# Kernel optimization log

Measured on AMD Instinct MI355X. Metric: run time of the kernel, lower is better.

## Reference

```python
import jax, jax.numpy as jnp
import numpy as np

B, T, D, N, K, H = 2, 2048, 2560, 8, 4, 256
G = N // K
WINDOW = 1024
ROPE_BASE = 10000
K_MASK = -2.3819763e+38
EPS = 1e-6


def apply_rope(inputs, positions, base_frequency):
    # inputs: [B, L, n, H]; positions: [B, L]
    head_dim = inputs.shape[-1]
    fraction = 2 * jnp.arange(0, head_dim // 2) / head_dim
    timescale = base_frequency ** fraction
    sinusoid = positions[..., None] / timescale[None, None, :]   # [B, L, H/2]
    sinusoid = sinusoid[..., None, :]                            # [B, L, 1, H/2]
    sin, cos = jnp.sin(sinusoid), jnp.cos(sinusoid)
    first, second = jnp.split(inputs, 2, axis=-1)
    out = jnp.concatenate([first * cos - second * sin,
                           second * cos + first * sin], axis=-1)
    return out.astype(inputs.dtype)


def rms_norm(x, scale):
    # Gemma-style RMSNorm: normalize over last dim, (1 + scale) gain.
    var = jnp.mean(jnp.square(x), axis=-1, keepdims=True)
    return x * jax.lax.rsqrt(var + EPS) * (1.0 + scale)


def setup_inputs() -> dict:
    key = jax.random.key(0)
    ks = jax.random.split(key, 5)
    x = jax.random.normal(ks[0], (B, T, D), jnp.float32)
    positions = jnp.broadcast_to(jnp.arange(T, dtype=jnp.int32), (B, T))
    # Causal sliding-window mask (LOCAL_SLIDING, window=1024), shape [B, 1, T, S].
    qp = jnp.arange(T)[:, None]
    kp = jnp.arange(T)[None, :]
    mask = (kp <= qp) & ((qp - kp) < WINDOW)
    attn_mask = jnp.broadcast_to(mask[None, None], (B, 1, T, T))
    q_w = jax.random.normal(ks[1], (N, D, H), jnp.float32) * 0.02
    kv_w = jax.random.normal(ks[2], (2, K, D, H), jnp.float32) * 0.02
    q_scale = jnp.zeros((H,), jnp.float32)
    k_scale = jnp.zeros((H,), jnp.float32)
    out_w = jax.random.normal(ks[3], (N, H, D), jnp.float32) * 0.02
    return {"x": x, "q_w": q_w, "kv_w": kv_w, "q_scale": q_scale,
            "k_scale": k_scale, "out_w": out_w,
            "positions": positions, "attn_mask": attn_mask}


def reference(x, q_w, kv_w, q_scale, k_scale, out_w, positions, attn_mask):
    dtype = x.dtype
    # GQA projections (num_kv_heads != num_heads branch)
    q = jnp.einsum('BTD,NDH->BTNH', x, q_w)          # [B,T,N,H]
    k = jnp.einsum('BSD,KDH->BSKH', x, kv_w[0])      # [B,S,K,H]
    v = jnp.einsum('BSD,KDH->BSKH', x, kv_w[1])      # [B,S,K,H]
    # QK-RMSNorm (GQA branch only)
    q = rms_norm(q, q_scale)
    k = rms_norm(k, k_scale)
    # RoPE + query scaling
    q = apply_rope(q, positions, ROPE_BASE)
    q = q * (H ** -0.5)
    k = apply_rope(k, positions, ROPE_BASE)
    # Grouped attention logits: [B,T,K,G,S] -> [B,T,N,S]
    qg = q.reshape(B, T, K, G, H)
    logits = jnp.einsum('BTKGH,BSKH->BTKGS', qg, k)
    logits = logits.reshape(B, T, N, T)
    # Mask + softmax (mask [B,1,T,S] -> [B,T,1,S])
    bmask = jnp.expand_dims(attn_mask.squeeze(axis=1), axis=2)
    masked = jnp.where(bmask, logits, K_MASK)
    probs = jax.nn.softmax(masked, axis=-1).astype(dtype)
    # Weighted values with grouped kv heads
    pg = probs.reshape(B, T, K, G, T)
    enc = jnp.einsum('BTKGS,BSKH->BTKGH', pg, v).reshape(B, T, N, H)
    out = jnp.einsum('BTNH,NHD->BTD', enc, out_w)
    return out
```

## Files before the change

### kernel.cpp

```cpp
#include <hip/hip_runtime.h>
#include <cstdint>

#define TB 2048
#define DIM 2560
#define NQ 8
#define NKV 4
#define HDIM 256
#define WIN 1024
#define KMASK -2.3819763e+38f

using f32x4 = __attribute__((ext_vector_type(4))) float;
using s16x8 = __attribute__((ext_vector_type(8))) short;
using u16x4 = __attribute__((ext_vector_type(4))) unsigned short;

__device__ __forceinline__ unsigned short f2bf(float f) {
  uint32_t x = __builtin_bit_cast(uint32_t, f);
  x += 0x7FFFu + ((x >> 16) & 1u);
  return (unsigned short)(x >> 16);
}

__device__ __forceinline__ float bf2f(unsigned short u) {
  uint32_t x = (uint32_t)u << 16;
  return __builtin_bit_cast(float, x);
}

__global__ __launch_bounds__(256) void k_prep(const float* __restrict__ q_w,
                                              const float* __restrict__ kv_w,
                                              const float* __restrict__ out_w,
                                              const float* __restrict__ x,
                                              unsigned short* __restrict__ W1,
                                              unsigned short* __restrict__ W3,
                                              unsigned short* __restrict__ XB) {
  __shared__ float tile[32][33];
  const int bi = blockIdx.x;
  const int tid = threadIdx.x;
  if (bi < 10240) {
    const int hd = bi / 640;
    const int rem = bi % 640;
    const int r0 = (rem / 8) * 32, c0 = (rem % 8) * 32;
    const float* src = (hd < 8) ? (q_w + (size_t)hd * DIM * HDIM)
                                : (kv_w + (size_t)(hd - 8) * DIM * HDIM);
    unsigned short* dst = W1 + (size_t)hd * HDIM * DIM;
    const int tx = tid & 31, ty = tid >> 5;
#pragma unroll
    for (int i = 0; i < 32; i += 8)
      tile[ty + i][tx] = src[(size_t)(r0 + ty + i) * HDIM + c0 + tx];
    __syncthreads();
#pragma unroll
    for (int i = 0; i < 32; i += 8)
      dst[(size_t)(c0 + ty + i) * DIM + r0 + tx] = f2bf(tile[tx][ty + i]);
  } else if (bi < 15360) {
    const int j = bi - 10240;
    const int c0 = (j % 80) * 32, r0 = (j / 80) * 32;
    const int tx = tid & 31, ty = tid >> 5;
#pragma unroll
    for (int i = 0; i < 32; i += 8)
      tile[ty + i][tx] = out_w[(size_t)(r0 + ty + i) * DIM + c0 + tx];
    __syncthreads();
#pragma unroll
    for (int i = 0; i < 32; i += 8)
      W3[(size_t)(c0 + ty + i) * 2048 + r0 + tx] = f2bf(tile[tx][ty + i]);
  } else {
    const int j = bi - 15360;
    int i = j * 256 + tid;
    f32x4 v = *(const f32x4*)&x[(size_t)i * 4];
    u16x4 o;
#pragma unroll
    for (int k = 0; k < 4; ++k) o[k] = f2bf(v[k]);
    *(u16x4*)&XB[(size_t)i * 4] = o;
  }
}

__global__ __launch_bounds__(512, 2) void k_gemm(const unsigned short* __restrict__ A,
                                                 const unsigned short* __restrict__ Bw,
                                                 void* __restrict__ Cc,
                                                 int Nc, int Kd, int nxl, int bf16out) {
  __shared__ unsigned short shA[2][256 * 64];
  __shared__ unsigned short shB[2][256 * 64];
  const int tid = threadIdx.x, w = tid >> 6, l = tid & 63;
  const int xcd = blockIdx.x & 7, loc = blockIdx.x >> 3;
  const int m0 = ((xcd >> 1) * 4 + loc / nxl) * 256;
  const int n0 = ((xcd & 1) * nxl + loc % nxl) * 256;

  const int srow = l >> 3;
  const int sw_colb = (((l & 7) ^ srow) << 4);
  const int wrow = w * 8;
  const int NT = Kd >> 6;

#define STG_A(buf, t, r)                                                                     \
  {                                                                                          \
    const char* src_ = (const char*)A +                                                      \
        ((size_t)(m0 + (r) * 64 + wrow + srow) * Kd + ((size_t)(t) << 6)) * 2 + sw_colb;     \
    __builtin_amdgcn_global_load_lds(                                                        \
        (__attribute__((address_space(1))) void*)src_,                                       \
        (__attribute__((address_space(3))) void*)((char*)&shA[buf][0] + (r) * 8192 + w * 1024), \
        16, 0, 0);                                                                           \
  }
#define STG_B(buf, t, r)                                                                     \
  {                                                                                          \
    const char* src_ = (const char*)Bw +                                                     \
        ((size_t)(n0 + (r) * 64 + wrow + srow) * Kd + ((size_t)(t) << 6)) * 2 + sw_colb;     \
    __builtin_amdgcn_global_load_lds(                                                        \
        (__attribute__((address_space(1))) void*)src_,                                       \
        (__attribute__((address_space(3))) void*)((char*)&shB[buf][0] + (r) * 8192 + w * 1024), \
        16, 0, 0);                                                                           \
  }

  const int wm = w >> 2, wn = w & 3;
  const int lr = l & 15, lg = l >> 4;
  const int rswz = (lr & 7) << 4;
  const int c0x = (lg * 16) ^ rswz;
  const int c1x = (64 + lg * 16) ^ rswz;
  f32x4 acc[8][4] = {};

#pragma unroll
  for (int r = 0; r < 4; ++r) { STG_A(0, 0, r); STG_B(0, 0, r); }
  asm volatile("s_waitcnt vmcnt(0)" ::: "memory");
  __builtin_amdgcn_s_barrier();

#pragma unroll 2
  for (int t = 0; t < NT; ++t) {
    const int buf = t & 1;
    const bool pf = (t + 1 < NT);
    const char* sa = (const char*)&shA[buf][0];
    const char* sb = (const char*)&shB[buf][0];
    s16x8 af[4], bf0[4], bf1[4];

#pragma unroll
    for (int mi = 0; mi < 4; ++mi)
      af[mi] = *(const s16x8*)(sa + (wm * 128 + mi * 16 + lr) * 128 + c0x);
#pragma unroll
    for (int ni = 0; ni < 4; ++ni)
      bf0[ni] = *(const s16x8*)(sb + (wn * 64 + ni * 16 + lr) * 128 + c0x);
    asm volatile("s_waitcnt vmcnt(0)" ::: "memory");
    if (pf) { STG_A(buf ^ 1, t + 1, 0); STG_A(buf ^ 1, t + 1, 2); }
    __builtin_amdgcn_s_barrier();
    asm volatile("s_waitcnt lgkmcnt(0)" ::: "memory");
    __builtin_amdgcn_s_setprio(1);
#pragma unroll
    for (int mi = 0; mi < 4; ++mi)
#pragma unroll
      for (int ni = 0; ni < 4; ++ni)
        acc[mi][ni] = __builtin_amdgcn_mfma_f32_16x16x32_bf16(af[mi], bf0[ni], acc[mi][ni], 0, 0, 0);
    __builtin_amdgcn_s_setprio(0);
    __builtin_amdgcn_s_barrier();

#pragma unroll
    for (int mi = 0; mi < 4; ++mi)
      af[mi] = *(const s16x8*)(sa + (wm * 128 + (4 + mi) * 16 + lr) * 128 + c0x);
    if (pf) { STG_B(buf ^ 1, t + 1, 0); STG_B(buf ^ 1, t + 1, 1); }
    __builtin_amdgcn_s_barrier();
    asm volatile("s_waitcnt lgkmcnt(0)" ::: "memory");
    __builtin_amdgcn_s_setprio(1);
#pragma unroll
    for (int mi = 0; mi < 4; ++mi)
#pragma unroll
      for (int ni = 0; ni < 4; ++ni)
        acc[4 + mi][ni] = __builtin_amdgcn_mfma_f32_16x16x32_bf16(af[mi], bf0[ni], acc[4 + mi][ni], 0, 0, 0);
    __builtin_amdgcn_s_setprio(0);
    __builtin_amdgcn_s_barrier();

#pragma unroll
    for (int mi = 0; mi < 4; ++mi)
      af[mi] = *(const s16x8*)(sa + (wm * 128 + mi * 16 + lr) * 128 + c1x);
#pragma unroll
    for (int ni = 0; ni < 4; ++ni)
      bf1[ni] = *(const s16x8*)(sb + (wn * 64 + ni * 16 + lr) * 128 + c1x);
    if (pf) { STG_B(buf ^ 1, t + 1, 2); STG_B(buf ^ 1, t + 1, 3); }
    __builtin_amdgcn_s_barrier();
    asm volatile("s_waitcnt lgkmcnt(0)" ::: "memory");
    __builtin_amdgcn_s_setprio(1);
#pragma unroll
    for (int mi = 0; mi < 4; ++mi)
#pragma unroll
      for (int ni = 0; ni < 4; ++ni)
        acc[mi][ni] = __builtin_amdgcn_mfma_f32_16x16x32_bf16(af[mi], bf1[ni], acc[mi][ni], 0, 0, 0);
    __builtin_amdgcn_s_setprio(0);
    __builtin_amdgcn_s_barrier();

#pragma unroll
    for (int mi = 0; mi < 4; ++mi)
      af[mi] = *(const s16x8*)(sa + (wm * 128 + (4 + mi) * 16 + lr) * 128 + c1x);
    if (pf) { STG_A(buf ^ 1, t + 1, 1); STG_A(buf ^ 1, t + 1, 3); }
    __builtin_amdgcn_s_barrier();
    asm volatile("s_waitcnt lgkmcnt(0)" ::: "memory");
    __builtin_amdgcn_s_setprio(1);
#pragma unroll
    for (int mi = 0; mi < 4; ++mi)
#pragma unroll
      for (int ni = 0; ni < 4; ++ni)
        acc[4 + mi][ni] = __builtin_amdgcn_mfma_f32_16x16x32_bf16(af[mi], bf1[ni], acc[4 + mi][ni], 0, 0, 0);
    __builtin_amdgcn_s_setprio(0);
    if (pf) {
      asm volatile("s_waitcnt vmcnt(2)" ::: "memory");
    } else {
      asm volatile("s_waitcnt vmcnt(0)" ::: "memory");
    }
    __builtin_amdgcn_s_barrier();
  }
#undef STG_A
#undef STG_B

  if (bf16out) {
    unsigned short* Co = (unsigned short*)Cc;
#pragma unroll
    for (int mi = 0; mi < 8; ++mi)
#pragma unroll
      for (int ni = 0; ni < 4; ++ni) {
        size_t base = (size_t)(m0 + wm * 128 + mi * 16 + lg * 4) * Nc + (n0 + wn * 64 + ni * 16 + lr);
#pragma unroll
        for (int i = 0; i < 4; ++i)
          Co[base + (size_t)i * Nc] = f2bf(acc[mi][ni][i]);
      }
  } else {
    float* Co = (float*)Cc;
#pragma unroll
    for (int mi = 0; mi < 8; ++mi)
#pragma unroll
      for (int ni = 0; ni < 4; ++ni) {
        size_t base = (size_t)(m0 + wm * 128 + mi * 16 + lg * 4) * Nc + (n0 + wn * 64 + ni * 16 + lr);
#pragma unroll
        for (int i = 0; i < 4; ++i)
          Co[base + (size_t)i * Nc] = acc[mi][ni][i];
      }
  }
}

__global__ __launch_bounds__(256) void k_post(const unsigned short* __restrict__ Y,
                                              const float* __restrict__ qsc,
                                              const float* __restrict__ ksc,
                                              const int* __restrict__ pos,
                                              unsigned short* __restrict__ Q,
                                              unsigned short* __restrict__ Kb,
                                              unsigned short* __restrict__ VT) {
  __shared__ float s_sin[128], s_cos[128];
  __shared__ unsigned short ttile[64][65];
  const int tid = threadIdx.x;
  if (blockIdx.x < 4096) {
    const int bt = blockIdx.x;
    const int b = bt >> 11, t = bt & (TB - 1);
    float p = (float)pos[bt];
    if (tid < 128) {
      float fr = (float)tid * (1.0f / 128.0f);
      float inv_ts = __expf(fr * -9.210340371976184f);
      float ang = p * inv_ts;
      float sv, cv;
      sincosf(ang, &sv, &cv);
      s_sin[tid] = sv;
      s_cos[tid] = cv;
    }
    __syncthreads();
    const int w = tid >> 6, l = tid & 63;
    const int jj0 = (l & 31) * 4;
    for (int sidx = w; sidx < 12; sidx += 4) {
      const unsigned short* src = Y + (size_t)bt * 4096 + sidx * 256;
      u16x4 vb = *(const u16x4*)&src[l * 4];
      float v[4];
#pragma unroll
      for (int j = 0; j < 4; ++j) v[j] = bf2f(vb[j]);
      float ss = v[0] * v[0] + v[1] * v[1] + v[2] * v[2] + v[3] * v[3];
#pragma unroll
      for (int d = 1; d < 64; d <<= 1) ss += __shfl_xor(ss, d);
      float rs = rsqrtf(ss * (1.0f / 256.0f) + 1e-6f);
      const float* scp = (sidx < 8) ? qsc : ksc;
      float nv[4], res[4];
#pragma unroll
      for (int j = 0; j < 4; ++j) nv[j] = v[j] * rs * (1.0f + scp[l * 4 + j]);
#pragma unroll
      for (int j = 0; j < 4; ++j) {
        float o = __shfl_xor(nv[j], 32);
        float sn = s_sin[jj0 + j], cs = s_cos[jj0 + j];
        res[j] = (l < 32) ? (nv[j] * cs - o * sn) : (nv[j] * cs + o * sn);
      }
      float qs = (sidx < 8) ? 0.0625f : 1.0f;
      u16x4 ob;
#pragma unroll
      for (int j = 0; j < 4; ++j) ob[j] = f2bf(res[j] * qs);
      if (sidx < 8) {
        size_t di = ((size_t)(b * NQ + sidx) * TB + t) * HDIM + l * 4;
        *(u16x4*)&Q[di] = ob;
      } else {
        size_t di = ((size_t)(b * NKV + (sidx - 8)) * TB + t) * HDIM + l * 4;
        *(u16x4*)&Kb[di] = ob;
      }
    }
  } else {
    const int zz = blockIdx.x - 4096;
    const int t0 = (zz & 31) * 64;
    const int h0 = ((zz >> 5) & 3) * 64;
    const int z = zz >> 7;
    const int bq = z >> 2, kh = z & 3;
#pragma unroll
    for (int rep = 0; rep < 16; ++rep) {
      int idx = rep * 256 + tid;
      int tr = idx >> 6, hc = idx & 63;
      ttile[tr][hc] = Y[(size_t)(bq * TB + t0 + tr) * 4096 + 3072 + kh * 256 + h0 + hc];
    }
    __syncthreads();
#pragma unroll
    for (int rep = 0; rep < 16; ++rep) {
      int idx = rep * 256 + tid;
      int hr = idx >> 6, tc = idx & 63;
      VT[((size_t)z * 256 + h0 + hr) * TB + t0 + tc] = ttile[tc][hr];
    }
  }
}

__global__ __launch_bounds__(256, 2) void k_attn(const unsigned short* __restrict__ Q,
                                                 const unsigned short* __restrict__ Kb,
                                                 const unsigned short* __restrict__ VT,
                                                 unsigned short* __restrict__ ENC) {
  __shared__ unsigned short shK[2][32 * 256];
  __shared__ unsigned short shV[2][256 * 32];
  __shared__ unsigned short Pb[4][16 * 40];
  const int tid = threadIdx.x, w = tid >> 6, l = tid & 63;
  const int bn = blockIdx.y;
  const int b = bn >> 3, n = bn & 7, kh = n >> 1;
  const int xr = blockIdx.x;
  const int xs = (xr & 1) ? (31 - (xr >> 1)) : (xr >> 1);
  const int t0b = xs * 64;
  const int t0 = t0b + w * 16;
  const int lr = l & 15, lg = l >> 4;
  const unsigned short* qp = Q + ((size_t)bn * TB + t0) * HDIM;
  const char* kbase = (const char*)(Kb + ((size_t)(b * NKV + kh) * TB) * HDIM);
  const char* vbase = (const char*)(VT + ((size_t)(b * NKV + kh) * HDIM) * TB);

  s16x8 aq[8];
#pragma unroll
  for (int kk = 0; kk < 8; ++kk)
    aq[kk] = *(const s16x8*)&qp[lr * HDIM + kk * 32 + lg * 8];

  f32x4 o[16] = {};
  float mrow[4], lsum[4];
#pragma unroll
  for (int i = 0; i < 4; ++i) { mrow[i] = -__builtin_inff(); lsum[i] = 0.f; }

  int lo = t0b - (WIN - 1);
  if (lo < 0) lo = 0;
  lo &= ~31;
  const int nsteps = (t0b + 32 - lo) / 32 + 1;

  const int k_row = (w << 1) + (l >> 5);
  const int k_colb = (l & 31) * 16;
  const int v_row = (w << 4) + (l >> 2);
  const int v_colb = (l & 3) * 16;
#define STAGE(buf, s0)                                                                       \
  {                                                                                          \
    _Pragma("unroll") for (int r = 0; r < 4; ++r) {                                          \
      int row = r * 8 + k_row;                                                               \
      int scol = k_colb ^ ((row & 7) << 4);                                                  \
      const char* src = kbase + (size_t)((s0) + row) * 512 + scol;                           \
      __builtin_amdgcn_global_load_lds(                                                      \
          (__attribute__((address_space(1))) void*)src,                                      \
          (__attribute__((address_space(3))) void*)((char*)&shK[buf][0] + r * 4096 + w * 1024), \
          16, 0, 0);                                                                         \
    }                                                                                        \
    _Pragma("unroll") for (int r = 0; r < 4; ++r) {                                          \
      int row = r * 64 + v_row;                                                              \
      const char* src = vbase + (size_t)row * (TB * 2) + (size_t)(s0) * 2 + v_colb;          \
      __builtin_amdgcn_global_load_lds(                                                      \
          (__attribute__((address_space(1))) void*)src,                                      \
          (__attribute__((address_space(3))) void*)((char*)&shV[buf][0] + r * 4096 + w * 1024), \
          16, 0, 0);                                                                         \
    }                                                                                        \
  }

  STAGE(0, lo);

  for (int step = 0; step < nsteps; ++step) {
    const int s0 = lo + step * 32;
    const int buf = step & 1;
    if (step + 1 < nsteps) {
      STAGE(buf ^ 1, s0 + 32);
      asm volatile("s_waitcnt vmcnt(8)" ::: "memory");
    } else {
      asm volatile("s_waitcnt vmcnt(0)" ::: "memory");
    }
    __builtin_amdgcn_s_barrier();

    const bool active = (s0 <= t0 + 15) && (s0 + 31 >= t0 - (WIN - 1));
    if (active) {
      f32x4 sacc[2] = {};
      const char* kt = (const char*)&shK[buf][0];
      const int swz = (lr & 7) << 4;
#pragma unroll
      for (int cb = 0; cb < 2; ++cb) {
        const int rb = (cb * 16 + lr) * 512;
        s16x8 bk[8];
#pragma unroll
        for (int kk = 0; kk < 8; ++kk)
          bk[kk] = *(const s16x8*)(kt + rb + ((kk * 64 + lg * 16) ^ swz));
        __builtin_amdgcn_s_setprio(1);
#pragma unroll
        for (int kk = 0; kk < 8; ++kk)
          sacc[cb] = __builtin_amdgcn_mfma_f32_16x16x32_bf16(aq[kk], bk[kk], sacc[cb], 0, 0, 0);
        __builtin_amdgcn_s_setprio(0);
      }
      float svA_[4], svB_[4];
      const bool nomask = (s0 + 31 <= t0) && (s0 >= t0 - (WIN - 16));
      if (nomask) {
#pragma unroll
        for (int i = 0; i < 4; ++i) { svA_[i] = sacc[0][i]; svB_[i] = sacc[1][i]; }
      } else {
#pragma unroll
        for (int i = 0; i < 4; ++i) {
          int trow = t0 + lg * 4 + i;
          int sA = s0 + lr, sB = s0 + 16 + lr;
          svA_[i] = ((sA <= trow) && (trow - sA < WIN)) ? sacc[0][i] : KMASK;
          svB_[i] = ((sB <= trow) && (trow - sB < WIN)) ? sacc[1][i] : KMASK;
        }
      }
      bool ok = true;
#pragma unroll
      for (int i = 0; i < 4; ++i)
        ok = ok && (svA_[i] <= mrow[i] + 8.f) && (svB_[i] <= mrow[i] + 8.f);
      if (!__all(ok)) {
        float r_[4];
#pragma unroll
        for (int i = 0; i < 4; ++i) {
          float mx = fmaxf(svA_[i], svB_[i]);
#pragma unroll
          for (int d = 1; d < 16; d <<= 1) mx = fmaxf(mx, __shfl_xor(mx, d));
          float mnew = fmaxf(mrow[i], mx);
          r_[i] = __expf(mrow[i] - mnew);
          lsum[i] *= r_[i];
          mrow[i] = mnew;
        }
#pragma unroll
        for (int hb = 0; hb < 16; ++hb)
#pragma unroll
          for (int i = 0; i < 4; ++i) o[hb][i] *= r_[i];
      }
#pragma unroll
      for (int i = 0; i < 4; ++i) {
        float pa = __expf(svA_[i] - mrow[i]);
        float pb = __expf(svB_[i] - mrow[i]);
        lsum[i] += pa + pb;
        int row = lg * 4 + i;
        Pb[w][row * 40 + lr] = f2bf(pa);
        Pb[w][row * 40 + 16 + lr] = f2bf(pb);
      }
      asm volatile("s_waitcnt lgkmcnt(0)" ::: "memory");
      s16x8 pfrag = *(const s16x8*)&Pb[w][lr * 40 + lg * 8];
      const char* vt = (const char*)&shV[buf][0];
      s16x8 vb[16];
#pragma unroll
      for (int hb = 0; hb < 16; ++hb)
        vb[hb] = *(const s16x8*)(vt + (hb * 16 + lr) * 64 + lg * 16);
      __builtin_amdgcn_s_setprio(1);
#pragma unroll
      for (int hb = 0; hb < 16; ++hb)
        o[hb] = __builtin_amdgcn_mfma_f32_16x16x32_bf16(pfrag, vb[hb], o[hb], 0, 0, 0);
      __builtin_amdgcn_s_setprio(0);
    }
    __builtin_amdgcn_s_barrier();
  }
#undef STAGE

#pragma unroll
  for (int i = 0; i < 4; ++i) {
    float s = lsum[i];
#pragma unroll
    for (int d = 1; d < 16; d <<= 1) s += __shfl_xor(s, d);
    lsum[i] = s;
  }
#pragma unroll
  for (int i = 0; i < 4; ++i) {
    int trow = t0 + lg * 4 + i;
    float inv = 1.0f / lsum[i];
    size_t rb = (size_t)(b * TB + trow) * 2048 + n * HDIM;
#pragma unroll
    for (int hb = 0; hb < 16; ++hb)
      ENC[rb + hb * 16 + lr] = f2bf(o[hb][i] * inv);
  }
}

extern "C" void kernel_launch(void* const* d_in, const int* in_sizes, int n_in,
                              void* d_out, int out_size, void* d_ws, size_t ws_size,
                              hipStream_t stream) {
  (void)in_sizes; (void)n_in; (void)out_size; (void)ws_size;
  const float* x = (const float*)d_in[0];
  const float* q_w = (const float*)d_in[1];
  const float* kv_w = (const float*)d_in[2];
  const float* qsc = (const float*)d_in[3];
  const float* ksc = (const float*)d_in[4];
  const float* out_w = (const float*)d_in[5];
  const int* pos = (const int*)d_in[6];
  float* out = (float*)d_out;

  char* ws = (char*)d_ws;
  unsigned short* W1 = (unsigned short*)(ws);
  unsigned short* W3 = (unsigned short*)(ws + 20971520);
  unsigned short* XB = (unsigned short*)(ws + 31457280);
  unsigned short* Y = (unsigned short*)(ws + 52428800);
  unsigned short* KB = (unsigned short*)(ws + 119537664);
  unsigned short* VT = (unsigned short*)(ws + 127926272);
  unsigned short* Qb = XB;
  unsigned short* ENC = (unsigned short*)(ws + 90000000);

  k_prep<<<dim3(25600), 256, 0, stream>>>(q_w, kv_w, out_w, x, W1, W3, XB);
  k_gemm<<<dim3(256), 512, 0, stream>>>(XB, W1, Y, 4096, DIM, 8, 1);
  k_post<<<dim3(5120), 256, 0, stream>>>(Y, qsc, ksc, pos, Qb, KB, VT);
  k_attn<<<dim3(32, 16), 256, 0, stream>>>(Qb, KB, VT, ENC);
  k_gemm<<<dim3(160), 512, 0, stream>>>(ENC, W3, out, DIM, 2048, 5, 0);
}
```

Before: 248.5 us.

## Use 16 waves per GEMM block with simpler double-buffered K loop

Doubles the GEMM block from 8 to 16 waves. Each wave now owns a 64x64 output tile instead of 128x64, which halves the accumulator registers. The hand-interleaved four-phase schedule, which staggered prefetches between MFMA groups, is replaced by a simple loop: prefetch the next K tile, wait, barrier, then compute two k-substeps. The goal is more latency hiding through more waves, at the cost of less per-wave data reuse, more LDS reads per MFMA, and losing the fine-grained overlap of loads and compute.

```diff
diff --git a/kernel.cpp b/kernel.cpp
--- a/kernel.cpp
+++ b/kernel.cpp
@@ -71,10 +71,10 @@
   }
 }
 
-__global__ __launch_bounds__(512, 2) void k_gemm(const unsigned short* __restrict__ A,
-                                                 const unsigned short* __restrict__ Bw,
-                                                 void* __restrict__ Cc,
-                                                 int Nc, int Kd, int nxl, int bf16out) {
+__global__ __launch_bounds__(1024, 4) void k_gemm(const unsigned short* __restrict__ A,
+                                                  const unsigned short* __restrict__ Bw,
+                                                  void* __restrict__ Cc,
+                                                  int Nc, int Kd, int nxl, int bf16out) {
   __shared__ unsigned short shA[2][256 * 64];
   __shared__ unsigned short shB[2][256 * 64];
   const int tid = threadIdx.x, w = tid >> 6, l = tid & 63;
@@ -82,132 +82,77 @@
   const int m0 = ((xcd >> 1) * 4 + loc / nxl) * 256;
   const int n0 = ((xcd & 1) * nxl + loc % nxl) * 256;
 
-  const int srow = l >> 3;
-  const int sw_colb = (((l & 7) ^ srow) << 4);
-  const int wrow = w * 8;
+  const int srow8 = l >> 3;
+  const int sw_colb = (((l & 7) ^ srow8) << 4);
   const int NT = Kd >> 6;
 
-#define STG_A(buf, t, r)                                                                     \
-  {                                                                                          \
-    const char* src_ = (const char*)A +                                                      \
-        ((size_t)(m0 + (r) * 64 + wrow + srow) * Kd + ((size_t)(t) << 6)) * 2 + sw_colb;     \
-    __builtin_amdgcn_global_load_lds(                                                        \
-        (__attribute__((address_space(1))) void*)src_,                                       \
-        (__attribute__((address_space(3))) void*)((char*)&shA[buf][0] + (r) * 8192 + w * 1024), \
-        16, 0, 0);                                                                           \
-  }
-#define STG_B(buf, t, r)                                                                     \
-  {                                                                                          \
-    const char* src_ = (const char*)Bw +                                                     \
-        ((size_t)(n0 + (r) * 64 + wrow + srow) * Kd + ((size_t)(t) << 6)) * 2 + sw_colb;     \
-    __builtin_amdgcn_global_load_lds(                                                        \
-        (__attribute__((address_space(1))) void*)src_,                                       \
-        (__attribute__((address_space(3))) void*)((char*)&shB[buf][0] + (r) * 8192 + w * 1024), \
-        16, 0, 0);                                                                           \
+#define GSTAGE(buf, t)                                                                      \
+  {                                                                                         \
+    const size_t kt = (size_t)(t) << 6;                                                     \
+    _Pragma("unroll") for (int i = 0; i < 2; ++i) {                                         \
+      const char* srcA = (const char*)A +                                                   \
+          ((size_t)(m0 + i * 128 + w * 8 + srow8) * Kd + kt) * 2 + sw_colb;                 \
+      __builtin_amdgcn_global_load_lds(                                                     \
+          (__attribute__((address_space(1))) void*)srcA,                                    \
+          (__attribute__((address_space(3))) void*)((char*)&shA[buf][0] + i * 16384 + w * 1024), \
+          16, 0, 0);                                                                        \
+      const char* srcB = (const char*)Bw +                                                  \
+          ((size_t)(n0 + i * 128 + w * 8 + srow8) * Kd + kt) * 2 + sw_colb;                 \
+      __builtin_amdgcn_global_load_lds(                                                     \
+          (__attribute__((address_space(1))) void*)srcB,                                    \
+          (__attribute__((address_space(3))) void*)((char*)&shB[buf][0] + i * 16384 + w * 1024), \
+          16, 0, 0);                                                                        \
+    }                                                                                       \
   }
 
   const int wm = w >> 2, wn = w & 3;
   const int lr = l & 15, lg = l >> 4;
   const int rswz = (lr & 7) << 4;
-  const int c0x = (lg * 16) ^ rswz;
-  const int c1x = (64 + lg * 16) ^ rswz;
-  f32x4 acc[8][4] = {};
-
-#pragma unroll
-  for (int r = 0; r < 4; ++r) { STG_A(0, 0, r); STG_B(0, 0, r); }
-  asm volatile("s_waitcnt vmcnt(0)" ::: "memory");
-  __builtin_amdgcn_s_barrier();
-
-#pragma unroll 2
+  f32x4 acc[4][4] = {};
+
+  GSTAGE(0, 0);
+
   for (int t = 0; t < NT; ++t) {
     const int buf = t & 1;
-    const bool pf = (t + 1 < NT);
+    if (t + 1 < NT) {
+      GSTAGE(buf ^ 1, t + 1);
+      asm volatile("s_waitcnt vmcnt(4)" ::: "memory");
+    } else {
+      asm volatile("s_waitcnt vmcnt(0)" ::: "memory");
+    }
+    __builtin_amdgcn_s_barrier();
+
     const char* sa = (const char*)&shA[buf][0];
     const char* sb = (const char*)&shB[buf][0];
-    s16x8 af[4], bf0[4], bf1[4];
-
-#pragma unroll
-    for (int mi = 0; mi < 4; ++mi)
-      af[mi] = *(const s16x8*)(sa + (wm * 128 + mi * 16 + lr) * 128 + c0x);
-#pragma unroll
-    for (int ni = 0; ni < 4; ++ni)
-      bf0[ni] = *(const s16x8*)(sb + (wn * 64 + ni * 16 + lr) * 128 + c0x);
-    asm volatile("s_waitcnt vmcnt(0)" ::: "memory");
-    if (pf) { STG_A(buf ^ 1, t + 1, 0); STG_A(buf ^ 1, t + 1, 2); }
+#pragma unroll
+    for (int kk = 0; kk < 2; ++kk) {
+      const int cbx = (kk * 64 + lg * 16) ^ rswz;
+      s16x8 af[4], bfr[4];
+#pragma unroll
+      for (int mi = 0; mi < 4; ++mi)
+        af[mi] = *(const s16x8*)(sa + (wm * 64 + mi * 16 + lr) * 128 + cbx);
+#pragma unroll
+      for (int ni = 0; ni < 4; ++ni)
+        bfr[ni] = *(const s16x8*)(sb + (wn * 64 + ni * 16 + lr) * 128 + cbx);
+      __builtin_amdgcn_s_setprio(1);
+#pragma unroll
+      for (int mi = 0; mi < 4; ++mi)
+#pragma unroll
+        for (int ni = 0; ni < 4; ++ni)
+          acc[mi][ni] = __builtin_amdgcn_mfma_f32_16x16x32_bf16(af[mi], bfr[ni], acc[mi][ni], 0, 0, 0);
+      __builtin_amdgcn_s_setprio(0);
+    }
     __builtin_amdgcn_s_barrier();
-    asm volatile("s_waitcnt lgkmcnt(0)" ::: "memory");
-    __builtin_amdgcn_s_setprio(1);
-#pragma unroll
-    for (int mi = 0; mi < 4; ++mi)
-#pragma unroll
-      for (int ni = 0; ni < 4; ++ni)
-        acc[mi][ni] = __builtin_amdgcn_mfma_f32_16x16x32_bf16(af[mi], bf0[ni], acc[mi][ni], 0, 0, 0);
-    __builtin_amdgcn_s_setprio(0);
-    __builtin_amdgcn_s_barrier();
-
-#pragma unroll
-    for (int mi = 0; mi < 4; ++mi)
-      af[mi] = *(const s16x8*)(sa + (wm * 128 + (4 + mi) * 16 + lr) * 128 + c0x);
-    if (pf) { STG_B(buf ^ 1, t + 1, 0); STG_B(buf ^ 1, t + 1, 1); }
-    __builtin_amdgcn_s_barrier();
-    asm volatile("s_waitcnt lgkmcnt(0)" ::: "memory");
-    __builtin_amdgcn_s_setprio(1);
-#pragma unroll
-    for (int mi = 0; mi < 4; ++mi)
-#pragma unroll
-      for (int ni = 0; ni < 4; ++ni)
-        acc[4 + mi][ni] = __builtin_amdgcn_mfma_f32_16x16x32_bf16(af[mi], bf0[ni], acc[4 + mi][ni], 0, 0, 0);
-    __builtin_amdgcn_s_setprio(0);
-    __builtin_amdgcn_s_barrier();
-
-#pragma unroll
-    for (int mi = 0; mi < 4; ++mi)
-      af[mi] = *(const s16x8*)(sa + (wm * 128 + mi * 16 + lr) * 128 + c1x);
-#pragma unroll
-    for (int ni = 0; ni < 4; ++ni)
-      bf1[ni] = *(const s16x8*)(sb + (wn * 64 + ni * 16 + lr) * 128 + c1x);
-    if (pf) { STG_B(buf ^ 1, t + 1, 2); STG_B(buf ^ 1, t + 1, 3); }
-    __builtin_amdgcn_s_barrier();
-    asm volatile("s_waitcnt lgkmcnt(0)" ::: "memory");
-    __builtin_amdgcn_s_setprio(1);
-#pragma unroll
-    for (int mi = 0; mi < 4; ++mi)
-#pragma unroll
-      for (int ni = 0; ni < 4; ++ni)
-        acc[mi][ni] = __builtin_amdgcn_mfma_f32_16x16x32_bf16(af[mi], bf1[ni], acc[mi][ni], 0, 0, 0);
-    __builtin_amdgcn_s_setprio(0);
-    __builtin_amdgcn_s_barrier();
-
-#pragma unroll
-    for (int mi = 0; mi < 4; ++mi)
-      af[mi] = *(const s16x8*)(sa + (wm * 128 + (4 + mi) * 16 + lr) * 128 + c1x);
-    if (pf) { STG_A(buf ^ 1, t + 1, 1); STG_A(buf ^ 1, t + 1, 3); }
-    __builtin_amdgcn_s_barrier();
-    asm volatile("s_waitcnt lgkmcnt(0)" ::: "memory");
-    __builtin_amdgcn_s_setprio(1);
-#pragma unroll
-    for (int mi = 0; mi < 4; ++mi)
-#pragma unroll
-      for (int ni = 0; ni < 4; ++ni)
-        acc[4 + mi][ni] = __builtin_amdgcn_mfma_f32_16x16x32_bf16(af[mi], bf1[ni], acc[4 + mi][ni], 0, 0, 0);
-    __builtin_amdgcn_s_setprio(0);
-    if (pf) {
-      asm volatile("s_waitcnt vmcnt(2)" ::: "memory");
-    } else {
-      asm volatile("s_waitcnt vmcnt(0)" ::: "memory");
-    }
-    __builtin_amdgcn_s_barrier();
-  }
-#undef STG_A
-#undef STG_B
+  }
+#undef GSTAGE
 
   if (bf16out) {
     unsigned short* Co = (unsigned short*)Cc;
 #pragma unroll
-    for (int mi = 0; mi < 8; ++mi)
+    for (int mi = 0; mi < 4; ++mi)
 #pragma unroll
       for (int ni = 0; ni < 4; ++ni) {
-        size_t base = (size_t)(m0 + wm * 128 + mi * 16 + lg * 4) * Nc + (n0 + wn * 64 + ni * 16 + lr);
+        size_t base = (size_t)(m0 + wm * 64 + mi * 16 + lg * 4) * Nc + (n0 + wn * 64 + ni * 16 + lr);
 #pragma unroll
         for (int i = 0; i < 4; ++i)
           Co[base + (size_t)i * Nc] = f2bf(acc[mi][ni][i]);
@@ -215,10 +160,10 @@
   } else {
     float* Co = (float*)Cc;
 #pragma unroll
-    for (int mi = 0; mi < 8; ++mi)
+    for (int mi = 0; mi < 4; ++mi)
 #pragma unroll
       for (int ni = 0; ni < 4; ++ni) {
-        size_t base = (size_t)(m0 + wm * 128 + mi * 16 + lg * 4) * Nc + (n0 + wn * 64 + ni * 16 + lr);
+        size_t base = (size_t)(m0 + wm * 64 + mi * 16 + lg * 4) * Nc + (n0 + wn * 64 + ni * 16 + lr);
 #pragma unroll
         for (int i = 0; i < 4; ++i)
           Co[base + (size_t)i * Nc] = acc[mi][ni][i];
@@ -499,8 +444,8 @@
   unsigned short* ENC = (unsigned short*)(ws + 90000000);
 
   k_prep<<<dim3(25600), 256, 0, stream>>>(q_w, kv_w, out_w, x, W1, W3, XB);
-  k_gemm<<<dim3(256), 512, 0, stream>>>(XB, W1, Y, 4096, DIM, 8, 1);
+  k_gemm<<<dim3(256), 1024, 0, stream>>>(XB, W1, Y, 4096, DIM, 8, 1);
   k_post<<<dim3(5120), 256, 0, stream>>>(Y, qsc, ksc, pos, Qb, KB, VT);
   k_attn<<<dim3(32, 16), 256, 0, stream>>>(Qb, KB, VT, ENC);
-  k_gemm<<<dim3(160), 512, 0, stream>>>(ENC, W3, out, DIM, 2048, 5, 0);
-}
+  k_gemm<<<dim3(160), 1024, 0, stream>>>(ENC, W3, out, DIM, 2048, 5, 0);
+}
```

New measurement: 246.2 us. No clear change (-1.0%).

## Add dedicated 256x160-tile output projection GEMM to fill all CUs

Applied to the files above, without the earlier changes.

Replaces the generic GEMM for the output projection (M=4096, N=2560, K=2048) with a specialised kernel that uses 256x160 tiles, giving 256 blocks instead of 160 so every CU gets work. The new kernel maps blocks to XCDs for L2 locality, uses a 2x4 wave layout with 4x5 MFMA fragments, and overlaps the next stage's global-to-LDS load with compute using partial vmcnt waits. It also drops the unroll-2 pragma on the generic GEMM's main loop. The cost is a kernel with hardcoded shapes and uneven B-tile loading across waves.

```diff
diff --git a/kernel.cpp b/kernel.cpp
--- a/kernel.cpp
+++ b/kernel.cpp
@@ -118,7 +118,6 @@
   asm volatile("s_waitcnt vmcnt(0)" ::: "memory");
   __builtin_amdgcn_s_barrier();
 
-#pragma unroll 2
   for (int t = 0; t < NT; ++t) {
     const int buf = t & 1;
     const bool pf = (t + 1 < NT);
@@ -224,6 +223,107 @@
           Co[base + (size_t)i * Nc] = acc[mi][ni][i];
       }
   }
+}
+
+__global__ __launch_bounds__(512, 2) void k_gemm3(const unsigned short* __restrict__ A,
+                                                  const unsigned short* __restrict__ Bw,
+                                                  float* __restrict__ Cc) {
+  const int Nc = 2560, Kd = 2048;
+  __shared__ unsigned short shA[2][256 * 64];
+  __shared__ unsigned short shB[2][160 * 64];
+  const int tid = threadIdx.x, w = tid >> 6, l = tid & 63;
+  const int xcd = blockIdx.x & 7, loc = blockIdx.x >> 3;
+  const int m0 = (xcd * 2 + (loc >> 4)) * 256;
+  const int n0 = (loc & 15) * 160;
+
+  const int srow = l >> 3;
+  const int sw_colb = (((l & 7) ^ srow) << 4);
+  const int wrow = w * 8;
+  const int NT = Kd >> 6;
+
+#define GSTAGE3(buf, t)                                                                     \
+  {                                                                                         \
+    const size_t kt = (size_t)(t) << 6;                                                     \
+    _Pragma("unroll") for (int r = 0; r < 4; ++r) {                                         \
+      const char* srcA = (const char*)A +                                                   \
+          ((size_t)(m0 + r * 64 + wrow + srow) * Kd + kt) * 2 + sw_colb;                    \
+      __builtin_amdgcn_global_load_lds(                                                     \
+          (__attribute__((address_space(1))) void*)srcA,                                    \
+          (__attribute__((address_space(3))) void*)((char*)&shA[buf][0] + r * 8192 + w * 1024), \
+          16, 0, 0);                                                                        \
+    }                                                                                       \
+    _Pragma("unroll") for (int r = 0; r < 2; ++r) {                                         \
+      const char* srcB = (const char*)Bw +                                                  \
+          ((size_t)(n0 + r * 64 + wrow + srow) * Kd + kt) * 2 + sw_colb;                    \
+      __builtin_amdgcn_global_load_lds(                                                     \
+          (__attribute__((address_space(1))) void*)srcB,                                    \
+          (__attribute__((address_space(3))) void*)((char*)&shB[buf][0] + r * 8192 + w * 1024), \
+          16, 0, 0);                                                                        \
+    }                                                                                       \
+    if (w < 4) {                                                                            \
+      const char* srcB = (const char*)Bw +                                                  \
+          ((size_t)(n0 + 128 + wrow + srow) * Kd + kt) * 2 + sw_colb;                       \
+      __builtin_amdgcn_global_load_lds(                                                     \
+          (__attribute__((address_space(1))) void*)srcB,                                    \
+          (__attribute__((address_space(3))) void*)((char*)&shB[buf][0] + 16384 + w * 1024), \
+          16, 0, 0);                                                                        \
+    }                                                                                       \
+  }
+
+  const int wm = w >> 1, wn = w & 1;
+  const int lr = l & 15, lg = l >> 4;
+  const int rswz = (lr & 7) << 4;
+  f32x4 acc[4][5] = {};
+
+  GSTAGE3(0, 0);
+
+  for (int t = 0; t < NT; ++t) {
+    const int buf = t & 1;
+    if (t + 1 < NT) {
+      GSTAGE3(buf ^ 1, t + 1);
+      if (w < 4) {
+        asm volatile("s_waitcnt vmcnt(7)" ::: "memory");
+      } else {
+        asm volatile("s_waitcnt vmcnt(6)" ::: "memory");
+      }
+    } else {
+      asm volatile("s_waitcnt vmcnt(0)" ::: "memory");
+    }
+    __builtin_amdgcn_s_barrier();
+
+    const char* sa = (const char*)&shA[buf][0];
+    const char* sb = (const char*)&shB[buf][0];
+#pragma unroll
+    for (int kk = 0; kk < 2; ++kk) {
+      const int cbx = (kk * 64 + lg * 16) ^ rswz;
+      s16x8 af[4], bfr[5];
+#pragma unroll
+      for (int mi = 0; mi < 4; ++mi)
+        af[mi] = *(const s16x8*)(sa + (wm * 64 + mi * 16 + lr) * 128 + cbx);
+#pragma unroll
+      for (int ni = 0; ni < 5; ++ni)
+        bfr[ni] = *(const s16x8*)(sb + (wn * 80 + ni * 16 + lr) * 128 + cbx);
+      __builtin_amdgcn_s_setprio(1);
+#pragma unroll
+      for (int mi = 0; mi < 4; ++mi)
+#pragma unroll
+        for (int ni = 0; ni < 5; ++ni)
+          acc[mi][ni] = __builtin_amdgcn_mfma_f32_16x16x32_bf16(af[mi], bfr[ni], acc[mi][ni], 0, 0, 0);
+      __builtin_amdgcn_s_setprio(0);
+    }
+    __builtin_amdgcn_s_barrier();
+  }
+#undef GSTAGE3
+
+#pragma unroll
+  for (int mi = 0; mi < 4; ++mi)
+#pragma unroll
+    for (int ni = 0; ni < 5; ++ni) {
+      size_t base = (size_t)(m0 + wm * 64 + mi * 16 + lg * 4) * Nc + (n0 + wn * 80 + ni * 16 + lr);
+#pragma unroll
+      for (int i = 0; i < 4; ++i)
+        Cc[base + (size_t)i * Nc] = acc[mi][ni][i];
+    }
 }
 
 __global__ __launch_bounds__(256) void k_post(const unsigned short* __restrict__ Y,
@@ -502,5 +602,5 @@
   k_gemm<<<dim3(256), 512, 0, stream>>>(XB, W1, Y, 4096, DIM, 8, 1);
   k_post<<<dim3(5120), 256, 0, stream>>>(Y, qsc, ksc, pos, Qb, KB, VT);
   k_attn<<<dim3(32, 16), 256, 0, stream>>>(Qb, KB, VT, ENC);
-  k_gemm<<<dim3(160), 512, 0, stream>>>(ENC, W3, out, DIM, 2048, 5, 0);
-}
+  k_gemm3<<<dim3(256), 512, 0, stream>>>(ENC, W3, out);
+}
```

Measured after the change: 241.4 us (median of 2 runs). 1.03x faster.
